# Kernel tuning notes

Measured on AMD Instinct MI355X. Metric: run time of the kernel, lower is better.

## Reference

```python
import jax, jax.numpy as jnp
import numpy as np

S = 32            # state: nodes per graph, conv output channels
B = 4096          # number of graphs
N = B * S         # total nodes
E = 2 * 1024 * 1024  # total edges (avg degree 16)
A = 2             # action_space_dimension
NACT = 32         # number_of_actions (adv heads)
EPS = 1e-5


def setup_inputs() -> dict:
    key = jax.random.key(0)
    ks = jax.random.split(key, 24)
    f = lambda k, sh, s: (jax.random.normal(k, sh, jnp.float32) * s)
    return {
        'x': f(ks[0], (N, 2), 1.0),
        'edge_index': jax.random.randint(ks[1], (2, E), 0, N),
        # conv1 MLP: Linear(4,16) -> ReLU -> Linear(16,S)
        'c1W1': f(ks[2], (4, 16), 0.5), 'c1b1': jnp.zeros((16,), jnp.float32),
        'c1W2': f(ks[3], (16, S), 0.25), 'c1b2': jnp.zeros((S,), jnp.float32),
        # conv2/conv3 MLPs: Linear(2*S,16) -> ReLU -> Linear(16,S)
        'c2W1': f(ks[4], (2 * S, 16), 0.12), 'c2b1': jnp.zeros((16,), jnp.float32),
        'c2W2': f(ks[5], (16, S), 0.25), 'c2b2': jnp.zeros((S,), jnp.float32),
        'c3W1': f(ks[6], (2 * S, 16), 0.12), 'c3b1': jnp.zeros((16,), jnp.float32),
        'c3W2': f(ks[7], (16, S), 0.25), 'c3b2': jnp.zeros((S,), jnp.float32),
        # 3 BatchNorm1d(S) layers (stacked)
        'bn_g': jnp.ones((3, S), jnp.float32), 'bn_b': jnp.zeros((3, S), jnp.float32),
        # dense head MLP 1024->256->256->256
        'mW1': f(ks[8], (S * S, 256), 0.03), 'mb1': jnp.zeros((256,), jnp.float32),
        'mW2': f(ks[9], (256, 256), 0.06), 'mb2': jnp.zeros((256,), jnp.float32),
        'mW3': f(ks[10], (256, 256), 0.06), 'mb3': jnp.zeros((256,), jnp.float32),
        # dueling heads
        'vW': f(ks[11], (256, 1), 0.06), 'vb': jnp.zeros((1,), jnp.float32),
        'aW': f(ks[12], (NACT, 256, A), 0.06), 'ab': jnp.zeros((NACT, A), jnp.float32),
    }


def _edgeconv(x, src, dst, W1, b1, W2, b2):
    # PyG EdgeConv with aggr='add': msg = MLP(cat[x_i, x_j - x_i]), summed at target i
    xi = x[dst]                       # [E, F]
    xj = x[src]                       # [E, F]
    m = jnp.concatenate([xi, xj - xi], axis=-1)        # [E, 2F]
    h = jnp.maximum(m @ W1 + b1, 0.0) @ W2 + b2        # [E, S]
    return jax.ops.segment_sum(h, dst, num_segments=x.shape[0])  # [N, S]


def _bn(h, g, b):
    # BatchNorm1d in training mode: batch stats over node dim, biased variance
    mu = h.mean(axis=0)
    var = jnp.mean((h - mu) ** 2, axis=0)
    return (h - mu) * jax.lax.rsqrt(var + EPS) * g + b


def reference(x, edge_index, c1W1, c1b1, c1W2, c1b2, c2W1, c2b1, c2W2, c2b2,
              c3W1, c3b1, c3W2, c3b2, bn_g, bn_b, mW1, mb1, mW2, mb2,
              mW3, mb3, vW, vb, aW, ab):
    src, dst = edge_index[0], edge_index[1]
    h = _edgeconv(x, src, dst, c1W1, c1b1, c1W2, c1b2)
    h = jax.nn.relu(_bn(h, bn_g[0], bn_b[0]))
    h = _edgeconv(h, src, dst, c2W1, c2b1, c2W2, c2b2)
    h = jax.nn.relu(_bn(h, bn_g[1], bn_b[1]))
    h = _edgeconv(h, src, dst, c3W1, c3b1, c3W2, c3b2)
    h = jax.nn.relu(_bn(h, bn_g[2], bn_b[2]))
    nb = x.shape[0] // S                                 # graphs in batch
    out = h.reshape(nb, S * S)                           # [B, in_size]
    out = jax.nn.relu(out @ mW1 + mb1)
    out = jax.nn.relu(out @ mW2 + mb2)
    out = jax.nn.relu(out @ mW3 + mb3)                   # [B, 256]
    value = out @ vW + vb                                # [B, 1]
    adv = jnp.einsum('bf,nfa->bna', out, aW) + ab        # [B, NACT, A]
    q = value[:, :, None] + adv - adv.mean(axis=2, keepdims=True)
    return q
```

## Files before the change

kernel.cpp:

```cpp
#include <hip/hip_runtime.h>
#include <hip/hip_fp16.h>

#define NN 131072
#define EE 2097152
#define SS 32
#define HH 16
#define BB 4096
#define EPS 1e-5f

#define BKT 512
#define BNODES 256
#define CAP 4864
#define SCAP 8192
#define TILE 8192

typedef _Float16 f16x8 __attribute__((ext_vector_type(8)));
typedef float f32x4 __attribute__((ext_vector_type(4)));

__global__ __launch_bounds__(1024) void k_bsort(const int* __restrict__ ei, int* __restrict__ gcount,
                                                int* __restrict__ words) {
    __shared__ int cnt[BKT];
    __shared__ int tstart[BKT];
    __shared__ int gshift[BKT];
    __shared__ int sc[BKT];
    __shared__ int sword[TILE];
    __shared__ int sdst[TILE];
    int t = threadIdx.x;
    if (t < BKT) cnt[t] = 0;
    __syncthreads();
    int e0 = blockIdx.x * TILE;
#pragma unroll
    for (int it = 0; it < TILE / 1024; ++it) {
        int dst = ei[EE + e0 + it * 1024 + t];
        atomicAdd(&cnt[dst >> 8], 1);
    }
    __syncthreads();
    int val = (t < BKT) ? cnt[t] : 0;
    if (t < BKT) sc[t] = val;
    __syncthreads();
    for (int d = 1; d < BKT; d <<= 1) {
        int v2 = (t >= d && t < BKT) ? sc[t - d] : 0;
        __syncthreads();
        if (t < BKT) sc[t] += v2;
        __syncthreads();
    }
    if (t < BKT) {
        int excl = sc[t] - val;
        tstart[t] = excl;
        gshift[t] = t * CAP + atomicAdd(&gcount[t], val) - excl;
        cnt[t] = 0;
    }
    __syncthreads();
#pragma unroll
    for (int it = 0; it < TILE / 1024; ++it) {
        int e = e0 + it * 1024 + t;
        int src = ei[e];
        int dst = ei[EE + e];
        int b = dst >> 8;
        int r = atomicAdd(&cnt[b], 1);
        int p = tstart[b] + r;
        sword[p] = src | ((dst & 255) << 17);
        sdst[p] = gshift[b] + p;
    }
    __syncthreads();
#pragma unroll
    for (int it = 0; it < TILE / 1024; ++it) {
        int i = it * 1024 + t;
        words[sdst[i]] = sword[i];
    }
}

__global__ __launch_bounds__(512) void k_csr(const int* __restrict__ words, const int* __restrict__ gcount,
                                             int* __restrict__ ssrc, int* __restrict__ offs,
                                             int* __restrict__ offe) {
    __shared__ int hist[BNODES];
    __shared__ int sc[BNODES];
    __shared__ int base[BNODES];
    int t = threadIdx.x;
    int b = blockIdx.x;
    if (t < BNODES) hist[t] = 0;
    __syncthreads();
    int cnt = gcount[b];
    const int* wp = words + (size_t)b * CAP;
    for (int p = t; p < cnt; p += 512) atomicAdd(&hist[wp[p] >> 17], 1);
    __syncthreads();
    int val = 0, pval = 0;
    if (t < BNODES) {
        val = hist[t];
        pval = (val + 15) & ~15;
        sc[t] = pval;
    }
    __syncthreads();
    for (int d = 1; d < BNODES; d <<= 1) {
        int v2 = (t >= d && t < BNODES) ? sc[t - d] : 0;
        __syncthreads();
        if (t < BNODES) sc[t] += v2;
        __syncthreads();
    }
    int gbase = b * SCAP;
    if (t < BNODES) {
        base[t] = sc[t] - pval;
        offs[b * BNODES + t] = gbase + base[t];
        offe[b * BNODES + t] = gbase + base[t] + val;
        hist[t] = 0;
    }
    __syncthreads();
    for (int p = t; p < cnt; p += 512) {
        int w = wp[p];
        int dl = w >> 17;
        int r = atomicAdd(&hist[dl], 1);
        ssrc[gbase + base[dl] + r] = w & 0x1FFFF;
    }
    if (t < BNODES) {
        int s = gbase + base[t];
        for (int i = val; i < pval; ++i) ssrc[s + i] = NN;
    }
}

__global__ __launch_bounds__(256) void k_prep(const float* __restrict__ mW1, const float* __restrict__ mW2,
                                              const float* __restrict__ mW3, const float* __restrict__ vW,
                                              const float* __restrict__ vb, const float* __restrict__ aW,
                                              const float* __restrict__ ab,
                                              _Float16* __restrict__ W1T, _Float16* __restrict__ W2T,
                                              _Float16* __restrict__ W3T, _Float16* __restrict__ BqT,
                                              float* __restrict__ biasq, int* __restrict__ gcount,
                                              float* __restrict__ bns) {
    int i = blockIdx.x * 256 + threadIdx.x;
    {
        int k = i >> 8, n = i & 255;
        W1T[(size_t)n * 1024 + k] = (_Float16)mW1[i];
    }
    if (i < 65536) {
        int k = i >> 8, n = i & 255;
        W2T[n * 256 + k] = (_Float16)mW2[i];
        W3T[n * 256 + k] = (_Float16)mW3[i];
    }
    if (i < 16384) {
        int f = i >> 6, j = i & 63;
        int n = j >> 1, a = j & 1;
        float wa = aW[n * 512 + f * 2 + a];
        float wo = aW[n * 512 + f * 2 + (1 - a)];
        BqT[j * 256 + f] = (_Float16)(vW[f] + 0.5f * (wa - wo));
    }
    if (i < 64) biasq[i] = vb[0] + 0.5f * (ab[i] - ab[i ^ 1]);
    if (i < 512) gcount[i] = 0;
    if (i < 192) bns[i] = 0.f;
}

__global__ __launch_bounds__(256) void k_pre1(const float* __restrict__ x, const float* __restrict__ W1,
                                              const float* __restrict__ b1, float* __restrict__ u,
                                              __half* __restrict__ v) {
    int t = blockIdx.x * 256 + threadIdx.x;
    int n = t >> 4, c = t & 15;
    float x0 = x[n * 2], x1 = x[n * 2 + 1];
    float w0 = W1[c], w1 = W1[16 + c], w2 = W1[32 + c], w3 = W1[48 + c];
    u[t] = b1[c] + x0 * (w0 - w2) + x1 * (w1 - w3);
    v[t] = __float2half(x0 * w2 + x1 * w3);
    if (blockIdx.x == 0 && t < 16) v[NN * 16 + t] = __float2half(-60000.0f);
}

__global__ __launch_bounds__(256) void k_bnpre(const float* __restrict__ y, const float* __restrict__ bns,
                                               const float* __restrict__ g, const float* __restrict__ bb,
                                               const float* __restrict__ W1, const float* __restrict__ b1,
                                               float* __restrict__ u, __half* __restrict__ v) {
    __shared__ float sh[16][33];
    __shared__ float wd[32][16];
    __shared__ float wv[32][16];
    __shared__ float scL[32], soL[32];
    int t = threadIdx.x;
    if (t < 32) {
        const float inv_n = 1.0f / (float)NN;
        float mean = bns[t] * inv_n;
        float var = bns[32 + t] * inv_n - mean * mean;
        float s = g[t] * rsqrtf(var + EPS);
        scL[t] = s;
        soL[t] = bb[t] - mean * s;
    }
    for (int i = t; i < 512; i += 256) {
        int f = i >> 4, c = i & 15;
        float wt = W1[i];
        float wb = W1[512 + i];
        wd[f][c] = wt - wb;
        wv[f][c] = wb;
    }
    __syncthreads();
    int nb = blockIdx.x * 16;
    for (int i = t; i < 512; i += 256) {
        int col = i & 31;
        sh[i >> 5][col] = fmaxf(y[nb * 32 + i] * scL[col] + soL[col], 0.f);
    }
    __syncthreads();
    int c = t & 15, nl = t >> 4;
    float uu = b1[c], vv = 0.f;
#pragma unroll
    for (int f = 0; f < 32; ++f) {
        float hv = sh[nl][f];
        uu += hv * wd[f][c];
        vv += hv * wv[f][c];
    }
    int n = nb + nl;
    u[n * 16 + c] = uu;
    v[n * 16 + c] = __float2half(vv);
    if (blockIdx.x == 0 && t < 16) v[NN * 16 + t] = __float2half(-60000.0f);
}

__global__ __launch_bounds__(256) void k_gather(const float* __restrict__ u, const __half* __restrict__ v,
                                                const int* __restrict__ ssrc, const int* __restrict__ offs,
                                                const int* __restrict__ offe,
                                                const float* __restrict__ W2, const float* __restrict__ b2,
                                                float* __restrict__ y) {
    __shared__ float sw2[512];
    __shared__ float sagg[32 * 18];
    __shared__ float cntL[32];
    int t = threadIdx.x;
    float w2a = W2[t], w2b = W2[t + 256];
    float b2r0 = b2[(t & 7) * 4], b2r1 = b2[(t & 7) * 4 + 1];
    float b2r2 = b2[(t & 7) * 4 + 2], b2r3 = b2[(t & 7) * 4 + 3];
    int nl = t >> 3, c2 = t & 7;
    int n = blockIdx.x * 32 + nl;
    int s0 = offs[n], e0 = offe[n];
    int pe = s0 + ((e0 - s0 + 15) & ~15);
    float2 uc = *(const float2*)(u + (size_t)n * 16 + 2 * c2);
    float a0 = 0.f, a1 = 0.f;
    for (int p = s0; p < pe; p += 16) {
        int idx[16];
#pragma unroll
        for (int i = 0; i < 16; ++i) idx[i] = ssrc[p + i];
        float2 vv[16];
#pragma unroll
        for (int i = 0; i < 16; ++i)
            vv[i] = __half22float2(*(const __half2*)(v + (size_t)idx[i] * 16 + 2 * c2));
#pragma unroll
        for (int i = 0; i < 16; ++i) {
            a0 += fmaxf(uc.x + vv[i].x, 0.f);
            a1 += fmaxf(uc.y + vv[i].y, 0.f);
        }
    }
    sagg[nl * 18 + 2 * c2] = a0;
    sagg[nl * 18 + 2 * c2 + 1] = a1;
    if (c2 == 0) cntL[nl] = (float)(e0 - s0);
    sw2[t] = w2a;
    sw2[t + 256] = w2b;
    __syncthreads();
    int node = t >> 3, oc = (t & 7) * 4;
    float cw = cntL[node];
    float o0 = b2r0 * cw, o1 = b2r1 * cw, o2 = b2r2 * cw, o3 = b2r3 * cw;
#pragma unroll
    for (int k = 0; k < 16; ++k) {
        float a = sagg[node * 18 + k];
        o0 += a * sw2[k * 32 + oc];
        o1 += a * sw2[k * 32 + oc + 1];
        o2 += a * sw2[k * 32 + oc + 2];
        o3 += a * sw2[k * 32 + oc + 3];
    }
    *(float4*)(y + (size_t)(blockIdx.x * 32 + node) * 32 + oc) = make_float4(o0, o1, o2, o3);
}

__global__ __launch_bounds__(256) void k_bnstat2(const float* __restrict__ y, float* __restrict__ bns) {
    __shared__ float ssm[8][33];
    __shared__ float ssq[8][33];
    int t = threadIdx.x;
    int c = t & 31, g = t >> 5;
    size_t r0 = (size_t)blockIdx.x * 512;
    float sm = 0.f, sq = 0.f;
    for (int i = 0; i < 64; ++i) {
        float val = y[(r0 + g + (size_t)i * 8) * 32 + c];
        sm += val;
        sq += val * val;
    }
    ssm[g][c] = sm;
    ssq[g][c] = sq;
    __syncthreads();
    if (t < 32) {
        float a = 0.f, bq = 0.f;
#pragma unroll
        for (int gg = 0; gg < 8; ++gg) { a += ssm[gg][t]; bq += ssq[gg][t]; }
        atomicAdd(&bns[t], a);
        atomicAdd(&bns[32 + t], bq);
    }
}

__global__ __launch_bounds__(256) void k_bnrelu16(const float* __restrict__ y, const float* __restrict__ bns,
                                                  const float* __restrict__ g, const float* __restrict__ bb,
                                                  _Float16* __restrict__ h16) {
    int t = blockIdx.x * 256 + threadIdx.x;
    int j = t & 31;
    const float inv_n = 1.0f / (float)NN;
    float mean = bns[j] * inv_n;
    float var = bns[32 + j] * inv_n - mean * mean;
    float sc = g[j] * rsqrtf(var + EPS);
    float sh = bb[j] - mean * sc;
    h16[t] = (_Float16)fmaxf(y[t] * sc + sh, 0.f);
}

__global__ __launch_bounds__(256) void k_mgemm(const _Float16* __restrict__ A, const _Float16* __restrict__ BT,
                                               const float* __restrict__ bias, float* __restrict__ Cf,
                                               _Float16* __restrict__ Ch, int M, int N, int K,
                                               int relu, int out16) {
    int tid = threadIdx.x;
    int w = tid >> 6, l = tid & 63, q = l >> 4, r = l & 15;
    int rowBase = blockIdx.x * 64;
    int col = blockIdx.y * 64 + w * 16 + r;
    const _Float16* ap = A + (size_t)(rowBase + r) * K + q * 8;
    const _Float16* bp = BT + (size_t)col * K + q * 8;
    f32x4 z = {0.f, 0.f, 0.f, 0.f};
    f32x4 acc[4] = {z, z, z, z};
    for (int k0 = 0; k0 < K; k0 += 32) {
        f16x8 bf = *(const f16x8*)(bp + k0);
        f16x8 a0 = *(const f16x8*)(ap + k0);
        f16x8 a1 = *(const f16x8*)(ap + k0 + (size_t)16 * K);
        f16x8 a2 = *(const f16x8*)(ap + k0 + (size_t)32 * K);
        f16x8 a3 = *(const f16x8*)(ap + k0 + (size_t)48 * K);
        acc[0] = __builtin_amdgcn_mfma_f32_16x16x32_f16(a0, bf, acc[0], 0, 0, 0);
        acc[1] = __builtin_amdgcn_mfma_f32_16x16x32_f16(a1, bf, acc[1], 0, 0, 0);
        acc[2] = __builtin_amdgcn_mfma_f32_16x16x32_f16(a2, bf, acc[2], 0, 0, 0);
        acc[3] = __builtin_amdgcn_mfma_f32_16x16x32_f16(a3, bf, acc[3], 0, 0, 0);
    }
    float bv = bias[col];
#pragma unroll
    for (int rt = 0; rt < 4; ++rt) {
#pragma unroll
        for (int i = 0; i < 4; ++i) {
            int row = rowBase + rt * 16 + q * 4 + i;
            float val = acc[rt][i] + bv;
            if (relu) val = fmaxf(val, 0.f);
            if (out16) Ch[(size_t)row * N + col] = (_Float16)val;
            else       Cf[(size_t)row * N + col] = val;
        }
    }
}

extern "C" void kernel_launch(void* const* d_in, const int* in_sizes, int n_in,
                              void* d_out, int out_size, void* d_ws, size_t ws_size,
                              hipStream_t stream) {
    const float* x    = (const float*)d_in[0];
    const int*   ei   = (const int*)d_in[1];
    const float* c1W1 = (const float*)d_in[2];
    const float* c1b1 = (const float*)d_in[3];
    const float* c1W2 = (const float*)d_in[4];
    const float* c1b2 = (const float*)d_in[5];
    const float* c2W1 = (const float*)d_in[6];
    const float* c2b1 = (const float*)d_in[7];
    const float* c2W2 = (const float*)d_in[8];
    const float* c2b2 = (const float*)d_in[9];
    const float* c3W1 = (const float*)d_in[10];
    const float* c3b1 = (const float*)d_in[11];
    const float* c3W2 = (const float*)d_in[12];
    const float* c3b2 = (const float*)d_in[13];
    const float* bn_g = (const float*)d_in[14];
    const float* bn_b = (const float*)d_in[15];
    const float* mW1  = (const float*)d_in[16];
    const float* mb1  = (const float*)d_in[17];
    const float* mW2  = (const float*)d_in[18];
    const float* mb2  = (const float*)d_in[19];
    const float* mW3  = (const float*)d_in[20];
    const float* mb3  = (const float*)d_in[21];
    const float* vW   = (const float*)d_in[22];
    const float* vb   = (const float*)d_in[23];
    const float* aW   = (const float*)d_in[24];
    const float* ab   = (const float*)d_in[25];
    float* out = (float*)d_out;

    char* p = (char*)d_ws;
    auto take = [&](size_t bytes) {
        char* r = p;
        p += (bytes + 255) & ~(size_t)255;
        return r;
    };
    int*       gcount = (int*)take((size_t)BKT * 4);
    int*       words  = (int*)take((size_t)BKT * CAP * 4);
    int*       ssrc   = (int*)take((size_t)BKT * SCAP * 4);
    int*       offs   = (int*)take((size_t)NN * 4);
    int*       offe   = (int*)take((size_t)NN * 4);
    float*     u      = (float*)take((size_t)NN * HH * 4);
    __half*    v      = (__half*)take((size_t)(NN + 1) * HH * 2);
    float*     y      = (float*)take((size_t)NN * SS * 4);
    _Float16*  h16    = (_Float16*)take((size_t)NN * SS * 2);
    float*     bns    = (float*)take(3 * 64 * 4);
    _Float16*  W1T    = (_Float16*)take((size_t)256 * 1024 * 2);
    _Float16*  W2T    = (_Float16*)take((size_t)256 * 256 * 2);
    _Float16*  W3T    = (_Float16*)take((size_t)256 * 256 * 2);
    _Float16*  BqT    = (_Float16*)take((size_t)64 * 256 * 2);
    float*     biasq  = (float*)take(64 * 4);
    _Float16*  Xa     = (_Float16*)take((size_t)BB * 256 * 2);
    _Float16*  Xb     = (_Float16*)take((size_t)BB * 256 * 2);

    k_prep<<<1024, 256, 0, stream>>>(mW1, mW2, mW3, vW, vb, aW, ab,
                                     W1T, W2T, W3T, BqT, biasq, gcount, bns);

    k_bsort<<<EE / TILE, 1024, 0, stream>>>(ei, gcount, words);
    k_csr<<<BKT, 512, 0, stream>>>(words, gcount, ssrc, offs, offe);

    k_pre1<<<NN * 16 / 256, 256, 0, stream>>>(x, c1W1, c1b1, u, v);
    k_gather<<<NN / 32, 256, 0, stream>>>(u, v, ssrc, offs, offe, c1W2, c1b2, y);
    k_bnstat2<<<256, 256, 0, stream>>>(y, bns);
    k_bnpre<<<NN / 16, 256, 0, stream>>>(y, bns, bn_g, bn_b, c2W1, c2b1, u, v);
    k_gather<<<NN / 32, 256, 0, stream>>>(u, v, ssrc, offs, offe, c2W2, c2b2, y);
    k_bnstat2<<<256, 256, 0, stream>>>(y, bns + 64);
    k_bnpre<<<NN / 16, 256, 0, stream>>>(y, bns + 64, bn_g + 32, bn_b + 32, c3W1, c3b1, u, v);
    k_gather<<<NN / 32, 256, 0, stream>>>(u, v, ssrc, offs, offe, c3W2, c3b2, y);
    k_bnstat2<<<256, 256, 0, stream>>>(y, bns + 128);
    k_bnrelu16<<<NN * 32 / 256, 256, 0, stream>>>(y, bns + 128, bn_g + 64, bn_b + 64, h16);

    k_mgemm<<<dim3(BB / 64, 4), 256, 0, stream>>>(h16, W1T, mb1, nullptr, Xa, BB, 256, 1024, 1, 1);
    k_mgemm<<<dim3(BB / 64, 4), 256, 0, stream>>>(Xa, W2T, mb2, nullptr, Xb, BB, 256, 256, 1, 1);
    k_mgemm<<<dim3(BB / 64, 4), 256, 0, stream>>>(Xb, W3T, mb3, nullptr, Xa, BB, 256, 256, 1, 1);
    k_mgemm<<<dim3(BB / 64, 1), 256, 0, stream>>>(Xa, BqT, biasq, out, nullptr, BB, 64, 256, 0, 0);
}
```

Baseline: 333.5 us.

## Gather half-rows with 16-byte loads and split edges across lanes in gather kernel

Changes how the gather kernel divides work among its 8 threads per node. Instead of each thread loading 4 bytes (two channels) from all 16 neighbor rows, each thread now loads a 16-byte half row (8 channels) from 4 of the 16 edges, and partial sums are combined with xor shuffles. This cuts the number of gather load instructions and per-thread index loads, at the cost of more accumulator registers and a shuffle reduction at the end.

```diff
diff --git a/kernel.cpp b/kernel.cpp
--- a/kernel.cpp
+++ b/kernel.cpp
@@ -216,29 +216,45 @@
     float w2a = W2[t], w2b = W2[t + 256];
     float b2r0 = b2[(t & 7) * 4], b2r1 = b2[(t & 7) * 4 + 1];
     float b2r2 = b2[(t & 7) * 4 + 2], b2r3 = b2[(t & 7) * 4 + 3];
-    int nl = t >> 3, c2 = t & 7;
+    int nl = t >> 3, s = t & 7;
+    int e2 = s >> 1;
+    int h = s & 1;
     int n = blockIdx.x * 32 + nl;
     int s0 = offs[n], e0 = offe[n];
     int pe = s0 + ((e0 - s0 + 15) & ~15);
-    float2 uc = *(const float2*)(u + (size_t)n * 16 + 2 * c2);
-    float a0 = 0.f, a1 = 0.f;
+    float ur[8];
+    *(float4*)&ur[0] = *(const float4*)(u + (size_t)n * 16 + h * 8);
+    *(float4*)&ur[4] = *(const float4*)(u + (size_t)n * 16 + h * 8 + 4);
+    float acc[8] = {};
     for (int p = s0; p < pe; p += 16) {
-        int idx[16];
-#pragma unroll
-        for (int i = 0; i < 16; ++i) idx[i] = ssrc[p + i];
-        float2 vv[16];
-#pragma unroll
-        for (int i = 0; i < 16; ++i)
-            vv[i] = __half22float2(*(const __half2*)(v + (size_t)idx[i] * 16 + 2 * c2));
-#pragma unroll
-        for (int i = 0; i < 16; ++i) {
-            a0 += fmaxf(uc.x + vv[i].x, 0.f);
-            a1 += fmaxf(uc.y + vv[i].y, 0.f);
+        int b0 = p + e2;
+        int i0 = ssrc[b0], i1 = ssrc[b0 + 4], i2 = ssrc[b0 + 8], i3 = ssrc[b0 + 12];
+        float4 r0 = ((const float4*)(v + (size_t)i0 * 16))[h];
+        float4 r1 = ((const float4*)(v + (size_t)i1 * 16))[h];
+        float4 r2 = ((const float4*)(v + (size_t)i2 * 16))[h];
+        float4 r3 = ((const float4*)(v + (size_t)i3 * 16))[h];
+        const float4* rs[4] = {&r0, &r1, &r2, &r3};
+#pragma unroll
+        for (int e = 0; e < 4; ++e) {
+            const __half2* hp = (const __half2*)rs[e];
+#pragma unroll
+            for (int k = 0; k < 4; ++k) {
+                float2 f = __half22float2(hp[k]);
+                acc[2 * k]     += fmaxf(ur[2 * k] + f.x, 0.f);
+                acc[2 * k + 1] += fmaxf(ur[2 * k + 1] + f.y, 0.f);
+            }
         }
     }
-    sagg[nl * 18 + 2 * c2] = a0;
-    sagg[nl * 18 + 2 * c2 + 1] = a1;
-    if (c2 == 0) cntL[nl] = (float)(e0 - s0);
+#pragma unroll
+    for (int j = 0; j < 8; ++j) {
+        acc[j] += __shfl_xor(acc[j], 2);
+        acc[j] += __shfl_xor(acc[j], 4);
+    }
+    if (e2 == 0) {
+#pragma unroll
+        for (int j = 0; j < 8; ++j) sagg[nl * 18 + h * 8 + j] = acc[j];
+    }
+    if (s == 0) cntL[nl] = (float)(e0 - s0);
     sw2[t] = w2a;
     sw2[t + 256] = w2b;
     __syncthreads();
```

New measurement: 333.5 us. About the same (+0.0%).
